# Performance work log

Hardware: AMD Instinct MI355X
Metric: run time of the kernel (lower is better)

The kernel has to match this reference:

```python
import jax, jax.numpy as jnp
import numpy as np

LEAKY_SLOPE = 0.2  # alpha in the torch module
EPS = 1e-10

N_NODES = 100000
N_EDGES = 1600000
IN_F = 128
OUT_F = 64


def setup_inputs() -> dict:
    key = jax.random.key(0)
    k1, k2, k3, k4, k5 = jax.random.split(key, 5)
    h = jax.random.normal(k1, (N_NODES, IN_F), dtype=jnp.float32)
    W = jax.random.normal(k2, (IN_F, OUT_F), dtype=jnp.float32) * (1.0 / np.sqrt(IN_F))
    a1 = jax.random.normal(k3, (OUT_F,), dtype=jnp.float32) * 0.1
    a2 = jax.random.normal(k4, (OUT_F,), dtype=jnp.float32) * 0.1
    edge_index = jax.random.randint(k5, (2, N_EDGES), 0, N_NODES, dtype=jnp.int32)
    return {"h": h, "W": W, "a1": a1, "a2": a2, "edge_index": edge_index}


def reference(h, W, a1, a2, edge_index):
    # h: [N, in_f], W: [in_f, out_f], a1/a2: [out_f], edge_index: [2, E]
    N = h.shape[0]
    Wh = h @ W                                   # [N, out_f]
    row, col = edge_index[0], edge_index[1]      # [E]
    f1 = Wh @ a1                                 # [N]
    f2 = Wh @ a2                                 # [N]
    e = jax.nn.leaky_relu(f1[row] + f2[col], negative_slope=LEAKY_SLOPE)  # [E]
    e_exp = jnp.exp(e - jnp.max(e))              # global-max shift, as in torch code
    exp_sum = jax.ops.segment_sum(e_exp, row, num_segments=N)            # [N]
    alpha = e_exp / (exp_sum[row] + EPS)         # [E]  (dropout is identity in eval)
    weighted_Wh = Wh[col] * alpha[:, None]       # [E, out_f]
    h_prime = jax.ops.segment_sum(weighted_Wh, row, num_segments=N)      # [N, out_f]
    return jax.nn.elu(h_prime)                   # concat=True path
```

## Files before the change

kernel.cpp:

```cpp
#include <hip/hip_runtime.h>
#include <hip/hip_bf16.h>

#define N_NODES 100000
#define N_EDGES 1600000
#define IN_F 128
#define OUT_F 64

#define RPB 64
#define NB  1563
#define C_CHUNKS 250
#define CHUNK 6400
#define M_CNT (NB * C_CHUNKS)
#define SCANA_BLOCKS ((M_CNT + 1023) / 1024)

typedef __attribute__((ext_vector_type(8))) short short8;
typedef __attribute__((ext_vector_type(4))) float f32x4;

#define LDS_PITCH 136

__device__ __forceinline__ unsigned short f2bf(float x) {
    unsigned u = __float_as_uint(x);
    return (unsigned short)((u + 0x7FFFu + ((u >> 16) & 1u)) >> 16);
}

__global__ __launch_bounds__(128) void k_wa(
    const float* __restrict__ W, const float* __restrict__ a1,
    const float* __restrict__ a2, float* __restrict__ wa1, float* __restrict__ wa2)
{
    const int k = threadIdx.x;
    float s1 = 0.f, s2 = 0.f;
    #pragma unroll 8
    for (int f = 0; f < OUT_F; f++) {
        const float w = W[k * OUT_F + f];
        s1 += w * a1[f];
        s2 += w * a2[f];
    }
    wa1[k] = s1;
    wa2[k] = s2;
}

__global__ __launch_bounds__(256) void k_gemm(
    const float* __restrict__ h, const float* __restrict__ W,
    const float* __restrict__ wa1, const float* __restrict__ wa2,
    float* __restrict__ Wh, float* __restrict__ f1, float* __restrict__ f2)
{
    __shared__ unsigned short Wt[OUT_F * LDS_PITCH];
    __shared__ unsigned short Al[16 * LDS_PITCH];

    const int tid  = threadIdx.x;
    const int lane = tid & 63;
    const int wav  = tid >> 6;
    const int quad = lane >> 4;
    const int nl   = lane & 15;

    for (int i = tid; i < IN_F * OUT_F; i += 256) {
        const int k = i >> 6, f = i & 63;
        Wt[f * LDS_PITCH + k] = f2bf(W[i]);
    }
    __syncthreads();

    short8 bfrag[4];
    #pragma unroll
    for (int ch = 0; ch < 4; ch++)
        bfrag[ch] = *(const short8*)&Wt[(wav * 16 + nl) * LDS_PITCH + ch * 32 + quad * 8];

    const int srow = tid >> 4;
    const int sc   = tid & 15;
    float w1r[8], w2r[8];
    #pragma unroll
    for (int j = 0; j < 8; j++) { w1r[j] = wa1[sc * 8 + j]; w2r[j] = wa2[sc * 8 + j]; }

    const int ntiles = N_NODES / 16;
    for (int tile = blockIdx.x; tile < ntiles; tile += gridDim.x) {
        const int base = tile * 16;
        __syncthreads();

        const float4 v0 = *(const float4*)&h[(base + srow) * IN_F + sc * 8];
        const float4 v1 = *(const float4*)&h[(base + srow) * IN_F + sc * 8 + 4];
        float p1 = v0.x * w1r[0] + v0.y * w1r[1] + v0.z * w1r[2] + v0.w * w1r[3]
                 + v1.x * w1r[4] + v1.y * w1r[5] + v1.z * w1r[6] + v1.w * w1r[7];
        float p2 = v0.x * w2r[0] + v0.y * w2r[1] + v0.z * w2r[2] + v0.w * w2r[3]
                 + v1.x * w2r[4] + v1.y * w2r[5] + v1.z * w2r[6] + v1.w * w2r[7];
        #pragma unroll
        for (int m = 8; m >= 1; m >>= 1) {
            p1 += __shfl_xor(p1, m, 64);
            p2 += __shfl_xor(p2, m, 64);
        }
        if (sc == 0) { f1[base + srow] = p1; f2[base + srow] = p2; }

        uint4 packed;
        packed.x = (unsigned)f2bf(v0.x) | ((unsigned)f2bf(v0.y) << 16);
        packed.y = (unsigned)f2bf(v0.z) | ((unsigned)f2bf(v0.w) << 16);
        packed.z = (unsigned)f2bf(v1.x) | ((unsigned)f2bf(v1.y) << 16);
        packed.w = (unsigned)f2bf(v1.z) | ((unsigned)f2bf(v1.w) << 16);
        *(uint4*)&Al[srow * LDS_PITCH + sc * 8] = packed;

        __syncthreads();

        f32x4 acc = {0.f, 0.f, 0.f, 0.f};
        #pragma unroll
        for (int ch = 0; ch < 4; ch++) {
            const short8 afrag = *(const short8*)&Al[nl * LDS_PITCH + ch * 32 + quad * 8];
            acc = __builtin_amdgcn_mfma_f32_16x16x32_bf16(afrag, bfrag[ch], acc, 0, 0, 0);
        }

        const int col = wav * 16 + nl;
        #pragma unroll
        for (int r = 0; r < 4; r++)
            Wh[(base + quad * 4 + r) * OUT_F + col] = acc[r];
    }
}

__global__ __launch_bounds__(1024) void k_hist(const int* __restrict__ ei,
                                               int* __restrict__ cnt)
{
    __shared__ int hl[NB];
    const int c = blockIdx.x;
    for (int i = threadIdx.x; i < NB; i += 1024) hl[i] = 0;
    __syncthreads();
    const int e0 = c * CHUNK;
    for (int i = threadIdx.x; i < CHUNK; i += 1024)
        atomicAdd(&hl[ei[e0 + i] >> 6], 1);
    __syncthreads();
    for (int b = threadIdx.x; b < NB; b += 1024)
        cnt[b * C_CHUNKS + c] = hl[b];
}

__global__ __launch_bounds__(256) void k_scanA(const int* __restrict__ cnt,
                                               int* __restrict__ bsum)
{
    __shared__ int sd[256];
    const int t = threadIdx.x;
    const int i0 = blockIdx.x * 1024 + t * 4;
    int s = 0;
    #pragma unroll
    for (int k = 0; k < 4; k++) {
        const int i = i0 + k;
        s += (i < M_CNT) ? cnt[i] : 0;
    }
    sd[t] = s; __syncthreads();
    for (int off = 128; off >= 1; off >>= 1) {
        if (t < off) sd[t] += sd[t + off];
        __syncthreads();
    }
    if (t == 0) bsum[blockIdx.x] = sd[0];
}

__global__ __launch_bounds__(512) void k_scanB(const int* __restrict__ bsum,
                                               int* __restrict__ bbase)
{
    __shared__ int s[512];
    const int t = threadIdx.x;
    const int mine = (t < SCANA_BLOCKS) ? bsum[t] : 0;
    s[t] = mine; __syncthreads();
    for (int off = 1; off < 512; off <<= 1) {
        const int v = (t >= off) ? s[t - off] : 0;
        __syncthreads();
        s[t] += v;
        __syncthreads();
    }
    if (t < SCANA_BLOCKS) bbase[t] = s[t] - mine;
}

__global__ __launch_bounds__(256) void k_scanC(int* __restrict__ cnt,
                                               const int* __restrict__ bbase)
{
    __shared__ int ts[256];
    const int t = threadIdx.x;
    const int i0 = blockIdx.x * 1024 + t * 4;
    int v[4]; int s = 0;
    #pragma unroll
    for (int k = 0; k < 4; k++) {
        const int i = i0 + k;
        v[k] = (i < M_CNT) ? cnt[i] : 0;
        s += v[k];
    }
    ts[t] = s; __syncthreads();
    for (int off = 1; off < 256; off <<= 1) {
        const int x = (t >= off) ? ts[t - off] : 0;
        __syncthreads();
        ts[t] += x;
        __syncthreads();
    }
    int excl = ts[t] - s + bbase[blockIdx.x];
    #pragma unroll
    for (int k = 0; k < 4; k++) {
        const int i = i0 + k;
        if (i < M_CNT) cnt[i] = excl;
        excl += v[k];
    }
}

__global__ __launch_bounds__(1024) void k_scatter(
    const int* __restrict__ ei,
    const float* __restrict__ f1,
    const float* __restrict__ f2,
    const int* __restrict__ cnt,
    uint2* __restrict__ pairs)
{
    __shared__ int cur[NB];
    const int c = blockIdx.x;
    for (int b = threadIdx.x; b < NB; b += 1024)
        cur[b] = cnt[b * C_CHUNKS + c];
    __syncthreads();

    const int e0 = c * CHUNK;
    for (int i = threadIdx.x; i < CHUNK; i += 1024) {
        const int r  = ei[e0 + i];
        const int cl = ei[N_EDGES + e0 + i];
        float x = f1[r] + f2[cl];
        x = (x >= 0.f) ? x : 0.2f * x;
        const float ee = __expf(x);
        const int pos = atomicAdd(&cur[r >> 6], 1);
        pairs[pos] = make_uint2(((unsigned)(r & 63) << 17) | (unsigned)cl,
                                __float_as_uint(ee));
    }
}

__global__ __launch_bounds__(256) void k_sort(
    const int* __restrict__ cnt,
    const uint2* __restrict__ pairs,
    uint2* __restrict__ pairs2,
    int* __restrict__ rowptr)
{
    __shared__ int cnt64[64];
    __shared__ int cur64[64];

    const int b   = blockIdx.x;
    const int tid = threadIdx.x;
    const int start = cnt[b * C_CHUNKS];
    const int end   = (b == NB - 1) ? N_EDGES : cnt[(b + 1) * C_CHUNKS];

    if (tid < 64) cnt64[tid] = 0;
    __syncthreads();

    for (int i = start + tid; i < end; i += 256)
        atomicAdd(&cnt64[pairs[i].x >> 17], 1);
    __syncthreads();

    if (tid < 64) {
        const int v = cnt64[tid];
        int s = v;
        #pragma unroll
        for (int off = 1; off < 64; off <<= 1) {
            const int x = __shfl_up(s, off, 64);
            if (tid >= off) s += x;
        }
        cur64[tid] = s - v;
        const int g = b * 64 + tid;
        if (g < N_NODES) rowptr[g] = start + s - v;
    }
    __syncthreads();

    for (int i = start + tid; i < end; i += 256) {
        const uint2 p = pairs[i];
        const int pos = atomicAdd(&cur64[p.x >> 17], 1);
        pairs2[start + pos] = p;
    }
    if (b == 0 && tid == 0) rowptr[N_NODES] = N_EDGES;
}

__global__ __launch_bounds__(256) void k_agg(
    const int* __restrict__ rowptr,
    const uint2* __restrict__ pairs2,
    const float* __restrict__ Wh,
    float* __restrict__ out)
{
    const int wid  = (blockIdx.x * 256 + threadIdx.x) >> 6;
    const int lane = threadIdx.x & 63;
    if (wid >= N_NODES) return;

    const int start = rowptr[wid];
    const int end   = rowptr[wid + 1];

    float acc = 0.f, s = 0.f;
    int j = start;
    for (; j + 4 <= end; j += 4) {
        const uint2 p0 = pairs2[j + 0];
        const uint2 p1 = pairs2[j + 1];
        const uint2 p2 = pairs2[j + 2];
        const uint2 p3 = pairs2[j + 3];
        const float w0 = Wh[((int)(p0.x & 0x1FFFFu) << 6) + lane];
        const float w1 = Wh[((int)(p1.x & 0x1FFFFu) << 6) + lane];
        const float w2 = Wh[((int)(p2.x & 0x1FFFFu) << 6) + lane];
        const float w3 = Wh[((int)(p3.x & 0x1FFFFu) << 6) + lane];
        const float e0 = __uint_as_float(p0.y);
        const float e1 = __uint_as_float(p1.y);
        const float e2 = __uint_as_float(p2.y);
        const float e3 = __uint_as_float(p3.y);
        acc += e0 * w0 + e1 * w1 + e2 * w2 + e3 * w3;
        s   += e0 + e1 + e2 + e3;
    }
    for (; j < end; j++) {
        const uint2 p = pairs2[j];
        const float ee = __uint_as_float(p.y);
        acc += ee * Wh[((int)(p.x & 0x1FFFFu) << 6) + lane];
        s   += ee;
    }

    const float r = acc / (s + 1e-10f);
    out[wid * OUT_F + lane] = (r > 0.f) ? r : expm1f(r);
}

extern "C" void kernel_launch(void* const* d_in, const int* in_sizes, int n_in,
                              void* d_out, int out_size, void* d_ws, size_t ws_size,
                              hipStream_t stream) {
    const float* h  = (const float*)d_in[0];
    const float* W  = (const float*)d_in[1];
    const float* a1 = (const float*)d_in[2];
    const float* a2 = (const float*)d_in[3];
    const int* ei   = (const int*)d_in[4];
    float* out      = (float*)d_out;

    float* ws     = (float*)d_ws;
    float* Wh     = ws;
    float* f1     = Wh + N_NODES * OUT_F;
    float* f2     = f1 + N_NODES;
    float* wa1    = f2 + N_NODES;
    float* wa2    = wa1 + 128;
    int*   cnt    = (int*)(wa2 + 128);
    int*   bsum   = cnt + M_CNT;
    int*   bbase  = bsum + 384;
    int*   rowptr = bbase + 384;
    int*   pad    = rowptr + 100002;
    if ((size_t)(pad - (int*)ws) & 1) pad++;
    uint2* pairs  = (uint2*)pad;
    uint2* pairs2 = pairs + N_EDGES;

    k_wa     <<<1, 128, 0, stream>>>(W, a1, a2, wa1, wa2);
    k_gemm   <<<1250, 256, 0, stream>>>(h, W, wa1, wa2, Wh, f1, f2);
    k_hist   <<<C_CHUNKS, 1024, 0, stream>>>(ei, cnt);
    k_scanA  <<<SCANA_BLOCKS, 256, 0, stream>>>(cnt, bsum);
    k_scanB  <<<1, 512, 0, stream>>>(bsum, bbase);
    k_scanC  <<<SCANA_BLOCKS, 256, 0, stream>>>(cnt, bbase);
    k_scatter<<<C_CHUNKS, 1024, 0, stream>>>(ei, f1, f2, cnt, pairs);
    k_sort   <<<NB, 256, 0, stream>>>(cnt, pairs, pairs2, rowptr);
    k_agg    <<<(N_NODES * 64 + 255) / 256, 256, 0, stream>>>(rowptr, pairs2, Wh, out);
}
```

Before: 253.8 us.

## Store Wh as bf16, fuse wa into hist, drop scanB, unroll agg by 8

The GEMM now writes Wh as bf16, so the gather in the aggregation kernel moves half the bytes per edge. The W·a projection is folded into the histogram kernel as an extra block. The separate single-block scan is removed, with each scanC block reducing its prefix of the block sums itself. The aggregation loop is unrolled by 8 with predication, and the launch count drops from nine to seven. This risks extra rounding error from bf16 Wh and adds redundant prefix reads in scanC.

```diff
diff --git a/kernel.cpp b/kernel.cpp
--- a/kernel.cpp
+++ b/kernel.cpp
@@ -23,26 +23,42 @@
     return (unsigned short)((u + 0x7FFFu + ((u >> 16) & 1u)) >> 16);
 }
 
-__global__ __launch_bounds__(128) void k_wa(
+__global__ __launch_bounds__(1024) void k_hist(
+    const int* __restrict__ ei, int* __restrict__ cnt,
     const float* __restrict__ W, const float* __restrict__ a1,
     const float* __restrict__ a2, float* __restrict__ wa1, float* __restrict__ wa2)
 {
-    const int k = threadIdx.x;
-    float s1 = 0.f, s2 = 0.f;
-    #pragma unroll 8
-    for (int f = 0; f < OUT_F; f++) {
-        const float w = W[k * OUT_F + f];
-        s1 += w * a1[f];
-        s2 += w * a2[f];
-    }
-    wa1[k] = s1;
-    wa2[k] = s2;
+    __shared__ int hl[NB];
+    const int c = blockIdx.x;
+    if (c == C_CHUNKS) {
+        const int k = threadIdx.x;
+        if (k < IN_F) {
+            float s1 = 0.f, s2 = 0.f;
+            #pragma unroll 8
+            for (int f = 0; f < OUT_F; f++) {
+                const float w = W[k * OUT_F + f];
+                s1 += w * a1[f];
+                s2 += w * a2[f];
+            }
+            wa1[k] = s1;
+            wa2[k] = s2;
+        }
+        return;
+    }
+    for (int i = threadIdx.x; i < NB; i += 1024) hl[i] = 0;
+    __syncthreads();
+    const int e0 = c * CHUNK;
+    for (int i = threadIdx.x; i < CHUNK; i += 1024)
+        atomicAdd(&hl[ei[e0 + i] >> 6], 1);
+    __syncthreads();
+    for (int b = threadIdx.x; b < NB; b += 1024)
+        cnt[b * C_CHUNKS + c] = hl[b];
 }
 
 __global__ __launch_bounds__(256) void k_gemm(
     const float* __restrict__ h, const float* __restrict__ W,
     const float* __restrict__ wa1, const float* __restrict__ wa2,
-    float* __restrict__ Wh, float* __restrict__ f1, float* __restrict__ f2)
+    unsigned short* __restrict__ Whb, float* __restrict__ f1, float* __restrict__ f2)
 {
     __shared__ unsigned short Wt[OUT_F * LDS_PITCH];
     __shared__ unsigned short Al[16 * LDS_PITCH];
@@ -107,23 +123,8 @@
         const int col = wav * 16 + nl;
         #pragma unroll
         for (int r = 0; r < 4; r++)
-            Wh[(base + quad * 4 + r) * OUT_F + col] = acc[r];
-    }
-}
-
-__global__ __launch_bounds__(1024) void k_hist(const int* __restrict__ ei,
-                                               int* __restrict__ cnt)
-{
-    __shared__ int hl[NB];
-    const int c = blockIdx.x;
-    for (int i = threadIdx.x; i < NB; i += 1024) hl[i] = 0;
-    __syncthreads();
-    const int e0 = c * CHUNK;
-    for (int i = threadIdx.x; i < CHUNK; i += 1024)
-        atomicAdd(&hl[ei[e0 + i] >> 6], 1);
-    __syncthreads();
-    for (int b = threadIdx.x; b < NB; b += 1024)
-        cnt[b * C_CHUNKS + c] = hl[b];
+            Whb[(base + quad * 4 + r) * OUT_F + col] = f2bf(acc[r]);
+    }
 }
 
 __global__ __launch_bounds__(256) void k_scanA(const int* __restrict__ cnt,
@@ -146,27 +147,22 @@
     if (t == 0) bsum[blockIdx.x] = sd[0];
 }
 
-__global__ __launch_bounds__(512) void k_scanB(const int* __restrict__ bsum,
-                                               int* __restrict__ bbase)
-{
-    __shared__ int s[512];
-    const int t = threadIdx.x;
-    const int mine = (t < SCANA_BLOCKS) ? bsum[t] : 0;
-    s[t] = mine; __syncthreads();
-    for (int off = 1; off < 512; off <<= 1) {
-        const int v = (t >= off) ? s[t - off] : 0;
-        __syncthreads();
-        s[t] += v;
-        __syncthreads();
-    }
-    if (t < SCANA_BLOCKS) bbase[t] = s[t] - mine;
-}
-
 __global__ __launch_bounds__(256) void k_scanC(int* __restrict__ cnt,
-                                               const int* __restrict__ bbase)
-{
+                                               const int* __restrict__ bsum)
+{
+    __shared__ int red[256];
     __shared__ int ts[256];
     const int t = threadIdx.x;
+
+    int pv = 0;
+    for (int i = t; i < (int)blockIdx.x; i += 256) pv += bsum[i];
+    red[t] = pv; __syncthreads();
+    for (int off = 128; off >= 1; off >>= 1) {
+        if (t < off) red[t] += red[t + off];
+        __syncthreads();
+    }
+    const int bpref = red[0];
+
     const int i0 = blockIdx.x * 1024 + t * 4;
     int v[4]; int s = 0;
     #pragma unroll
@@ -182,7 +178,7 @@
         ts[t] += x;
         __syncthreads();
     }
-    int excl = ts[t] - s + bbase[blockIdx.x];
+    int excl = ts[t] - s + bpref;
     #pragma unroll
     for (int k = 0; k < 4; k++) {
         const int i = i0 + k;
@@ -263,7 +259,7 @@
 __global__ __launch_bounds__(256) void k_agg(
     const int* __restrict__ rowptr,
     const uint2* __restrict__ pairs2,
-    const float* __restrict__ Wh,
+    const unsigned short* __restrict__ Whb,
     float* __restrict__ out)
 {
     const int wid  = (blockIdx.x * 256 + threadIdx.x) >> 6;
@@ -274,28 +270,18 @@
     const int end   = rowptr[wid + 1];
 
     float acc = 0.f, s = 0.f;
-    int j = start;
-    for (; j + 4 <= end; j += 4) {
-        const uint2 p0 = pairs2[j + 0];
-        const uint2 p1 = pairs2[j + 1];
-        const uint2 p2 = pairs2[j + 2];
-        const uint2 p3 = pairs2[j + 3];
-        const float w0 = Wh[((int)(p0.x & 0x1FFFFu) << 6) + lane];
-        const float w1 = Wh[((int)(p1.x & 0x1FFFFu) << 6) + lane];
-        const float w2 = Wh[((int)(p2.x & 0x1FFFFu) << 6) + lane];
-        const float w3 = Wh[((int)(p3.x & 0x1FFFFu) << 6) + lane];
-        const float e0 = __uint_as_float(p0.y);
-        const float e1 = __uint_as_float(p1.y);
-        const float e2 = __uint_as_float(p2.y);
-        const float e3 = __uint_as_float(p3.y);
-        acc += e0 * w0 + e1 * w1 + e2 * w2 + e3 * w3;
-        s   += e0 + e1 + e2 + e3;
-    }
-    for (; j < end; j++) {
-        const uint2 p = pairs2[j];
-        const float ee = __uint_as_float(p.y);
-        acc += ee * Wh[((int)(p.x & 0x1FFFFu) << 6) + lane];
-        s   += ee;
+    for (int j = start; j < end; j += 8) {
+        #pragma unroll
+        for (int k = 0; k < 8; k++) {
+            const int  jj = j + k;
+            const bool v  = jj < end;
+            const uint2 p = pairs2[v ? jj : start];
+            const float ee = v ? __uint_as_float(p.y) : 0.f;
+            const float wh = __uint_as_float(
+                (unsigned)Whb[(((int)(p.x & 0x1FFFFu)) << 6) + lane] << 16);
+            acc += ee * wh;
+            s   += ee;
+        }
     }
 
     const float r = acc / (s + 1e-10f);
@@ -312,28 +298,25 @@
     const int* ei   = (const int*)d_in[4];
     float* out      = (float*)d_out;
 
-    float* ws     = (float*)d_ws;
-    float* Wh     = ws;
-    float* f1     = Wh + N_NODES * OUT_F;
+    float* ws = (float*)d_ws;
+    unsigned short* Whb = (unsigned short*)ws;
+    float* f1     = ws + 3200000;
     float* f2     = f1 + N_NODES;
     float* wa1    = f2 + N_NODES;
     float* wa2    = wa1 + 128;
     int*   cnt    = (int*)(wa2 + 128);
     int*   bsum   = cnt + M_CNT;
-    int*   bbase  = bsum + 384;
-    int*   rowptr = bbase + 384;
+    int*   rowptr = bsum + 384;
     int*   pad    = rowptr + 100002;
     if ((size_t)(pad - (int*)ws) & 1) pad++;
     uint2* pairs  = (uint2*)pad;
     uint2* pairs2 = pairs + N_EDGES;
 
-    k_wa     <<<1, 128, 0, stream>>>(W, a1, a2, wa1, wa2);
-    k_gemm   <<<1250, 256, 0, stream>>>(h, W, wa1, wa2, Wh, f1, f2);
-    k_hist   <<<C_CHUNKS, 1024, 0, stream>>>(ei, cnt);
+    k_hist   <<<C_CHUNKS + 1, 1024, 0, stream>>>(ei, cnt, W, a1, a2, wa1, wa2);
     k_scanA  <<<SCANA_BLOCKS, 256, 0, stream>>>(cnt, bsum);
-    k_scanB  <<<1, 512, 0, stream>>>(bsum, bbase);
-    k_scanC  <<<SCANA_BLOCKS, 256, 0, stream>>>(cnt, bbase);
+    k_scanC  <<<SCANA_BLOCKS, 256, 0, stream>>>(cnt, bsum);
+    k_gemm   <<<1250, 256, 0, stream>>>(h, W, wa1, wa2, Whb, f1, f2);
     k_scatter<<<C_CHUNKS, 1024, 0, stream>>>(ei, f1, f2, cnt, pairs);
     k_sort   <<<NB, 256, 0, stream>>>(cnt, pairs, pairs2, rowptr);
-    k_agg    <<<(N_NODES * 64 + 255) / 256, 256, 0, stream>>>(rowptr, pairs2, Wh, out);
-}
+    k_agg    <<<(N_NODES * 64 + 255) / 256, 256, 0, stream>>>(rowptr, pairs2, Whb, out);
+}
```

New measurement: 281.7 us. +11.0%, slower.
